# Kernel tuning notes

Hardware: AMD Instinct MI355X
Metric: run time of the kernel (lower is better)

The kernel has to match this reference:

```python
import jax, jax.numpy as jnp
import numpy as np

N_NODES = 100000
N_EDGES = 1600000
S_FEAT = 16   # static node features
D_FEAT = 8    # dynamic node features
E_FEAT = 4    # edge features
K = 2
EDGE_IN = E_FEAT + 2 * S_FEAT + 2 * D_FEAT  # 52
HIDDEN = 2 * D_FEAT                          # 16


def setup_inputs() -> dict:
    key = jax.random.key(0)
    ks = jax.random.split(key, 12)
    inp = {
        "x_s": jax.random.normal(ks[0], (N_NODES, S_FEAT), jnp.float32),
        "x_d": jax.random.normal(ks[1], (N_NODES, D_FEAT), jnp.float32),
        "edge_attr": jax.random.normal(ks[2], (N_EDGES, E_FEAT), jnp.float32),
        # edge MLP: Linear(EDGE_IN->HIDDEN) + ReLU + Linear(HIDDEN->D_FEAT)
        "W1": jax.random.normal(ks[3], (HIDDEN, EDGE_IN), jnp.float32) / np.sqrt(EDGE_IN),
        "b1": jnp.zeros((HIDDEN,), jnp.float32),
        "W2": jax.random.normal(ks[4], (D_FEAT, HIDDEN), jnp.float32) / np.sqrt(HIDDEN),
        "b2": jnp.zeros((D_FEAT,), jnp.float32),
        # K+1 = 3 filter matrices, Linear(D->D, bias=False): y = x @ W.T
        "Wf0": jax.random.normal(ks[5], (D_FEAT, D_FEAT), jnp.float32) / np.sqrt(D_FEAT),
        "Wf1": jax.random.normal(ks[6], (D_FEAT, D_FEAT), jnp.float32) / np.sqrt(D_FEAT),
        "Wf2": jax.random.normal(ks[7], (D_FEAT, D_FEAT), jnp.float32) / np.sqrt(D_FEAT),
        "edge_index": jax.random.randint(ks[8], (2, N_EDGES), 0, N_NODES, jnp.int64
                                         if jax.config.jax_enable_x64 else jnp.int32),
    }
    return inp


def _edge_mlp(e, W1, b1, W2, b2):
    h = jax.nn.relu(e @ W1.T + b1)
    return h @ W2.T + b2


def reference(x_s, x_d, edge_attr, W1, b1, W2, b2, Wf0, Wf1, Wf2, edge_index):
    row, col = edge_index[0], edge_index[1]
    num_nodes = x_d.shape[0]

    # s_ij depends only on static inputs (x_s, x_d, edge_attr), not on `out`,
    # so it is identical across the K steps; compute it once. The per-step
    # boolean edge mask is applied multiplicatively below, which matches the
    # torch masked-gather/scatter exactly (normalization is per-edge).
    e_ij = jnp.concatenate(
        [x_s[row], x_s[col], x_d[row], x_d[col], edge_attr], axis=1)  # [E, 52]
    s_ij = _edge_mlp(e_ij, W1, b1, W2, b2)                            # [E, D]
    nrm = jnp.linalg.norm(s_ij, axis=1, keepdims=True)
    s_ij = jnp.where(nrm > 0, s_ij / jnp.where(nrm > 0, nrm, 1.0), 0.0)

    filters = [Wf0, Wf1, Wf2]
    out = x_d @ filters[0].T
    for k in range(K):
        mask = out.sum(1) != 0                         # [N]
        edge_mask = (mask[row] | mask[col]).astype(out.dtype)  # [E]
        hydraulic_gradient = out[col] - out[row]       # [E, D]
        shift_sum = hydraulic_gradient * s_ij * edge_mask[:, None]
        scattered = jax.ops.segment_sum(shift_sum, col, num_segments=num_nodes)
        scattered = scattered @ filters[k + 1].T
        out = out + scattered
    return out
```

## Files before the change

### kernel.cpp

```cpp
#include <hip/hip_runtime.h>
#include <hip/hip_fp16.h>

#define S_FEAT 16
#define D_FEAT 8
#define E_FEAT 4
#define EDGE_IN 52
#define HIDDEN 16
#define SCAN_CHUNK 2048
#define NSUB 8

typedef unsigned int uint4v __attribute__((ext_vector_type(4)));

__device__ __forceinline__ void mlp_sij(
    const float* __restrict__ x_s, const float* __restrict__ x_d,
    const float* __restrict__ edge_attr,
    const float* __restrict__ W1, const float* __restrict__ b1,
    const float* __restrict__ W2, const float* __restrict__ b2,
    int row, int col, int e, float s[D_FEAT])
{
    float in[EDGE_IN];
    {
        const float4* p = (const float4*)(x_s + (size_t)row * S_FEAT);
#pragma unroll
        for (int q = 0; q < 4; ++q) {
            float4 v = p[q];
            in[q * 4 + 0] = v.x; in[q * 4 + 1] = v.y;
            in[q * 4 + 2] = v.z; in[q * 4 + 3] = v.w;
        }
    }
    {
        const float4* p = (const float4*)(x_s + (size_t)col * S_FEAT);
#pragma unroll
        for (int q = 0; q < 4; ++q) {
            float4 v = p[q];
            in[16 + q * 4 + 0] = v.x; in[16 + q * 4 + 1] = v.y;
            in[16 + q * 4 + 2] = v.z; in[16 + q * 4 + 3] = v.w;
        }
    }
    {
        const float4* p = (const float4*)(x_d + (size_t)row * D_FEAT);
#pragma unroll
        for (int q = 0; q < 2; ++q) {
            float4 v = p[q];
            in[32 + q * 4 + 0] = v.x; in[32 + q * 4 + 1] = v.y;
            in[32 + q * 4 + 2] = v.z; in[32 + q * 4 + 3] = v.w;
        }
    }
    {
        const float4* p = (const float4*)(x_d + (size_t)col * D_FEAT);
#pragma unroll
        for (int q = 0; q < 2; ++q) {
            float4 v = p[q];
            in[40 + q * 4 + 0] = v.x; in[40 + q * 4 + 1] = v.y;
            in[40 + q * 4 + 2] = v.z; in[40 + q * 4 + 3] = v.w;
        }
    }
    {
        float4 v = *(const float4*)(edge_attr + (size_t)e * E_FEAT);
        in[48] = v.x; in[49] = v.y; in[50] = v.z; in[51] = v.w;
    }

    float h[HIDDEN];
#pragma unroll
    for (int i = 0; i < HIDDEN; ++i) {
        float acc = b1[i];
#pragma unroll
        for (int j = 0; j < EDGE_IN; ++j)
            acc = fmaf(in[j], W1[i * EDGE_IN + j], acc);
        h[i] = acc > 0.f ? acc : 0.f;
    }

    float nrm2 = 0.f;
#pragma unroll
    for (int i = 0; i < D_FEAT; ++i) {
        float acc = b2[i];
#pragma unroll
        for (int j = 0; j < HIDDEN; ++j)
            acc = fmaf(h[j], W2[i * HIDDEN + j], acc);
        s[i] = acc;
        nrm2 = fmaf(acc, acc, nrm2);
    }
    float nrm = sqrtf(nrm2);
    float inv = nrm > 0.f ? 1.f / nrm : 0.f;
#pragma unroll
    for (int i = 0; i < D_FEAT; ++i) s[i] *= inv;
}

__device__ __forceinline__ uint4v pack_rec(const float s[8], int row)
{
    int q[8];
#pragma unroll
    for (int i = 0; i < 8; ++i) {
        float v = fminf(fmaxf(s[i] * 2047.f, -2047.f), 2047.f);
        q[i] = (int)rintf(v) & 0xFFF;
    }
    uint4v r;
    r[0] = (unsigned)(q[0] | (q[1] << 12) | (q[2] << 24));
    r[1] = (unsigned)((q[2] >> 8) | (q[3] << 4) | (q[4] << 16) | (q[5] << 28));
    r[2] = (unsigned)((q[5] >> 4) | (q[6] << 8) | (q[7] << 20));
    r[3] = (unsigned)row;
    return r;
}

__device__ __forceinline__ float rec_s(uint4v r, int f)
{
    int off = f * 12;
    unsigned lo = off < 32 ? r[0] : (off < 64 ? r[1] : r[2]);
    unsigned hi = off < 32 ? r[1] : (off < 64 ? r[2] : 0u);
    unsigned sh = (unsigned)off & 31u;
    unsigned long long both = ((unsigned long long)hi << 32) | lo;
    int q = ((int)((unsigned)(both >> sh) << 20)) >> 20;
    return (float)q * (1.f / 2047.f);
}

__device__ __forceinline__ void unpack8h(uint4v w, float* dst)
{
#pragma unroll
    for (int i = 0; i < 4; ++i) {
        unsigned u = w[i];
        __half2 h;
        h = *reinterpret_cast<__half2*>(&u);
        float2 f = __half22float2(h);
        dst[2 * i] = f.x; dst[2 * i + 1] = f.y;
    }
}

__global__ __launch_bounds__(256) void zero_counts_kernel(int* __restrict__ counts, int M)
{
    int i = blockIdx.x * blockDim.x + threadIdx.x;
    if (i < M) counts[i] = 0;
}

__global__ __launch_bounds__(256) void hist_kernel(
    const int* __restrict__ ei, int E, int N, int* __restrict__ counts8)
{
    int e = blockIdx.x * blockDim.x + threadIdx.x;
    if (e >= E) return;
    int col = ei[E + e];
    atomicAdd(&counts8[(threadIdx.x & (NSUB - 1)) * N + col], 1);
}

__global__ __launch_bounds__(256) void scan_local_kernel(
    const int* __restrict__ counts8, int* __restrict__ partial,
    int* __restrict__ blocksums, int N)
{
    __shared__ int sh[256];
    int b = blockIdx.x, t = threadIdx.x;
    int base = b * SCAN_CHUNK + t * 8;
    int v[8];
    int run = 0;
#pragma unroll
    for (int j = 0; j < 8; ++j) {
        int c = 0;
        if (base + j < N) {
#pragma unroll
            for (int s8 = 0; s8 < NSUB; ++s8)
                c += counts8[s8 * N + base + j];
        }
        v[j] = run;
        run += c;
    }
    sh[t] = run;
    __syncthreads();
#pragma unroll
    for (int st = 1; st < 256; st <<= 1) {
        int x = (t >= st) ? sh[t - st] : 0;
        __syncthreads();
        sh[t] += x;
        __syncthreads();
    }
    int excl = sh[t] - run;
    if (t == 255) blocksums[b] = sh[255];
#pragma unroll
    for (int j = 0; j < 8; ++j)
        if (base + j < N) partial[base + j] = excl + v[j];
}

__global__ __launch_bounds__(64) void scan_blk_kernel(int* __restrict__ bs, int NB)
{
    int lane = threadIdx.x;
    int carry = 0;
    for (int base = 0; base < NB; base += 64) {
        int i = base + lane;
        int orig = (i < NB) ? bs[i] : 0;
        int v = orig;
#pragma unroll
        for (int st = 1; st < 64; st <<= 1) {
            int t = __shfl_up(v, st);
            if (lane >= st) v += t;
        }
        if (i < NB) bs[i] = carry + v - orig;
        carry += __shfl(v, 63);
    }
}

__global__ __launch_bounds__(256) void scan_add_kernel(
    int* __restrict__ offsets, int* __restrict__ cursor,
    const int* __restrict__ blocksums, int N, int E)
{
    int i = blockIdx.x * blockDim.x + threadIdx.x;
    if (i < N) {
        int off = offsets[i] + blocksums[i / SCAN_CHUNK];
        offsets[i] = off;
        cursor[i]  = off;
    } else if (i == N) {
        offsets[N] = E;
    }
}

__global__ __launch_bounds__(256) void proj_init_kernel(
    const float* __restrict__ x_s, const float* __restrict__ x_d,
    const float* __restrict__ W1, const float* __restrict__ b1,
    const float* __restrict__ Wf0,
    __half* __restrict__ PRh, __half* __restrict__ PCh,
    float* __restrict__ out, float* __restrict__ S, int N)
{
    int n = blockIdx.x * blockDim.x + threadIdx.x;
    if (n >= N) return;
    float xs[S_FEAT], xd[D_FEAT];
    {
        const float4* p = (const float4*)(x_s + (size_t)n * S_FEAT);
#pragma unroll
        for (int q = 0; q < 4; ++q) {
            float4 v = p[q];
            xs[q * 4 + 0] = v.x; xs[q * 4 + 1] = v.y;
            xs[q * 4 + 2] = v.z; xs[q * 4 + 3] = v.w;
        }
        const float4* pd = (const float4*)(x_d + (size_t)n * D_FEAT);
        float4 a = pd[0], b = pd[1];
        xd[0] = a.x; xd[1] = a.y; xd[2] = a.z; xd[3] = a.w;
        xd[4] = b.x; xd[5] = b.y; xd[6] = b.z; xd[7] = b.w;
    }
    __half prh[HIDDEN], pch[HIDDEN];
#pragma unroll
    for (int i = 0; i < HIDDEN; ++i) {
        const float* w = W1 + i * EDGE_IN;
        float a = b1[i], c = 0.f;
#pragma unroll
        for (int j = 0; j < S_FEAT; ++j) {
            a = fmaf(xs[j], w[j], a);
            c = fmaf(xs[j], w[16 + j], c);
        }
#pragma unroll
        for (int j = 0; j < D_FEAT; ++j) {
            a = fmaf(xd[j], w[32 + j], a);
            c = fmaf(xd[j], w[40 + j], c);
        }
        prh[i] = __float2half_rn(a);
        pch[i] = __float2half_rn(c);
    }
    {
        uint4v* pr = (uint4v*)(PRh + (size_t)n * HIDDEN);
        uint4v* pc = (uint4v*)(PCh + (size_t)n * HIDDEN);
        pr[0] = *(uint4v*)&prh[0]; pr[1] = *(uint4v*)&prh[8];
        pc[0] = *(uint4v*)&pch[0]; pc[1] = *(uint4v*)&pch[8];
    }
    float o[D_FEAT];
    float rs = 0.f;
#pragma unroll
    for (int i = 0; i < D_FEAT; ++i) {
        float acc = 0.f;
#pragma unroll
        for (int j = 0; j < D_FEAT; ++j)
            acc = fmaf(xd[j], Wf0[i * D_FEAT + j], acc);
        o[i] = acc;
        rs += acc;
    }
    float4* op = (float4*)(out + (size_t)n * D_FEAT);
    op[0] = make_float4(o[0], o[1], o[2], o[3]);
    op[1] = make_float4(o[4], o[5], o[6], o[7]);
    S[n] = rs;
}

__global__ __launch_bounds__(256) void mlp_scatter_proj_kernel(
    const __half* __restrict__ PRh, const __half* __restrict__ PCh,
    const float* __restrict__ edge_attr,
    const float* __restrict__ W1,
    const float* __restrict__ W2, const float* __restrict__ b2,
    const int* __restrict__ ei, int E,
    int* __restrict__ cursor, uint4v* __restrict__ recs)
{
    int e = blockIdx.x * blockDim.x + threadIdx.x;
    if (e >= E) return;
    int row = ei[e], col = ei[E + e];

    float pr[HIDDEN], pc[HIDDEN];
    {
        const uint4v* p = (const uint4v*)(PRh + (size_t)row * HIDDEN);
        const uint4v* c = (const uint4v*)(PCh + (size_t)col * HIDDEN);
        uint4v p0 = p[0], p1 = p[1], c0 = c[0], c1 = c[1];
        unpack8h(p0, pr); unpack8h(p1, pr + 8);
        unpack8h(c0, pc); unpack8h(c1, pc + 8);
    }
    float4 ea = *(const float4*)(edge_attr + (size_t)e * E_FEAT);

    float h[HIDDEN];
#pragma unroll
    for (int i = 0; i < HIDDEN; ++i) {
        const float* w = W1 + i * EDGE_IN + 48;
        float acc = pr[i] + pc[i];
        acc = fmaf(ea.x, w[0], acc);
        acc = fmaf(ea.y, w[1], acc);
        acc = fmaf(ea.z, w[2], acc);
        acc = fmaf(ea.w, w[3], acc);
        h[i] = acc > 0.f ? acc : 0.f;
    }

    float s[D_FEAT];
    float nrm2 = 0.f;
#pragma unroll
    for (int i = 0; i < D_FEAT; ++i) {
        float acc = b2[i];
#pragma unroll
        for (int j = 0; j < HIDDEN; ++j)
            acc = fmaf(h[j], W2[i * HIDDEN + j], acc);
        s[i] = acc;
        nrm2 = fmaf(acc, acc, nrm2);
    }
    float nrm = sqrtf(nrm2);
    float inv = nrm > 0.f ? 1.f / nrm : 0.f;
#pragma unroll
    for (int i = 0; i < D_FEAT; ++i) s[i] *= inv;

    uint4v rec = pack_rec(s, row);
    int pos = atomicAdd(&cursor[col], 1);
    __builtin_nontemporal_store(rec, recs + pos);
}

__global__ __launch_bounds__(256) void mlp_scatter_direct_kernel(
    const float* __restrict__ x_s, const float* __restrict__ x_d,
    const float* __restrict__ edge_attr,
    const float* __restrict__ W1, const float* __restrict__ b1,
    const float* __restrict__ W2, const float* __restrict__ b2,
    const int* __restrict__ ei, int E,
    int* __restrict__ cursor, uint4v* __restrict__ recs)
{
    int e = blockIdx.x * blockDim.x + threadIdx.x;
    if (e >= E) return;
    int row = ei[e], col = ei[E + e];
    float s[D_FEAT];
    mlp_sij(x_s, x_d, edge_attr, W1, b1, W2, b2, row, col, e, s);
    uint4v rec = pack_rec(s, row);
    int pos = atomicAdd(&cursor[col], 1);
    __builtin_nontemporal_store(rec, recs + pos);
}

__global__ __launch_bounds__(256) void node_init_kernel(
    const float* __restrict__ x_d, const float* __restrict__ Wf0,
    float* __restrict__ out, float* __restrict__ S, int N)
{
    int n = blockIdx.x * blockDim.x + threadIdx.x;
    if (n >= N) return;
    float xd[D_FEAT];
    const float4* p = (const float4*)(x_d + (size_t)n * D_FEAT);
    float4 a = p[0], b = p[1];
    xd[0] = a.x; xd[1] = a.y; xd[2] = a.z; xd[3] = a.w;
    xd[4] = b.x; xd[5] = b.y; xd[6] = b.z; xd[7] = b.w;
    float o[D_FEAT];
    float rs = 0.f;
#pragma unroll
    for (int i = 0; i < D_FEAT; ++i) {
        float acc = 0.f;
#pragma unroll
        for (int j = 0; j < D_FEAT; ++j)
            acc = fmaf(xd[j], Wf0[i * D_FEAT + j], acc);
        o[i] = acc;
        rs += acc;
    }
    float4* op = (float4*)(out + (size_t)n * D_FEAT);
    op[0] = make_float4(o[0], o[1], o[2], o[3]);
    op[1] = make_float4(o[4], o[5], o[6], o[7]);
    S[n] = rs;
}

__global__ __launch_bounds__(256) void csr_step_kernel(
    const float* __restrict__ out_in, float* __restrict__ out_out,
    const float* __restrict__ S_in, float* __restrict__ S_out,
    const int* __restrict__ offsets, const uint4v* __restrict__ recs,
    const float* __restrict__ Wf, int N)
{
    int lane = threadIdx.x & 63;
    int node = blockIdx.x * 4 + (threadIdx.x >> 6);
    if (node >= N) return;
    int e_sub = lane >> 3, f = lane & 7;
    int beg = offsets[node], end = offsets[node + 1];
    float outc = out_in[(size_t)node * 8 + f];
    bool mc = (S_in[node] != 0.f);
    float acc = 0.f;
    for (int base = beg; base < end; base += 8) {
        int e = base + e_sub;
        bool valid = e < end;
        uint4v rec = (uint4v)(0u);
        if (valid) rec = __builtin_nontemporal_load(recs + e);
        int row = (int)rec[3];
        float s = rec_s(rec, f);
        float outr = out_in[(size_t)row * 8 + f];
        bool m = mc || (S_in[row] != 0.f);
        acc += m ? (outc - outr) * s : 0.f;
    }
    acc += __shfl_xor(acc, 8);
    acc += __shfl_xor(acc, 16);
    acc += __shfl_xor(acc, 32);
    float upd = 0.f;
#pragma unroll
    for (int j = 0; j < 8; ++j) {
        float aj = __shfl(acc, (lane & ~7) | j);
        upd = fmaf(Wf[f * 8 + j], aj, upd);
    }
    float o = outc + upd;
    float rs = o;
    rs += __shfl_xor(rs, 1);
    rs += __shfl_xor(rs, 2);
    rs += __shfl_xor(rs, 4);
    if (e_sub == 0) {
        out_out[(size_t)node * 8 + f] = o;
        if (f == 0) S_out[node] = rs;
    }
}

__global__ __launch_bounds__(256) void fb_node_init_kernel(
    const float* __restrict__ x_d, const float* __restrict__ Wf0,
    float* __restrict__ out, float* __restrict__ scattered, int N)
{
    int n = blockIdx.x * blockDim.x + threadIdx.x;
    if (n >= N) return;
    float xd[D_FEAT];
    const float4* p = (const float4*)(x_d + (size_t)n * D_FEAT);
    float4 a = p[0], b = p[1];
    xd[0] = a.x; xd[1] = a.y; xd[2] = a.z; xd[3] = a.w;
    xd[4] = b.x; xd[5] = b.y; xd[6] = b.z; xd[7] = b.w;
    float o[D_FEAT];
#pragma unroll
    for (int i = 0; i < D_FEAT; ++i) {
        float acc = 0.f;
#pragma unroll
        for (int j = 0; j < D_FEAT; ++j)
            acc = fmaf(xd[j], Wf0[i * D_FEAT + j], acc);
        o[i] = acc;
    }
    float4* op = (float4*)(out + (size_t)n * D_FEAT);
    op[0] = make_float4(o[0], o[1], o[2], o[3]);
    op[1] = make_float4(o[4], o[5], o[6], o[7]);
    float4* sp = (float4*)(scattered + (size_t)n * D_FEAT);
    sp[0] = make_float4(0.f, 0.f, 0.f, 0.f);
    sp[1] = make_float4(0.f, 0.f, 0.f, 0.f);
}

__global__ __launch_bounds__(256) void fb_edge_step_kernel(
    const float* __restrict__ x_s, const float* __restrict__ x_d,
    const float* __restrict__ edge_attr,
    const float* __restrict__ W1, const float* __restrict__ b1,
    const float* __restrict__ W2, const float* __restrict__ b2,
    const float* __restrict__ out,
    const int* __restrict__ ei, int E, float* __restrict__ scattered)
{
    int e = blockIdx.x * blockDim.x + threadIdx.x;
    if (e >= E) return;
    int row = ei[e], col = ei[E + e];
    const float4* pr = (const float4*)(out + (size_t)row * D_FEAT);
    const float4* pc = (const float4*)(out + (size_t)col * D_FEAT);
    float4 r0 = pr[0], r1 = pr[1], c0 = pc[0], c1 = pc[1];
    float srow = r0.x + r0.y + r0.z + r0.w + r1.x + r1.y + r1.z + r1.w;
    float scol = c0.x + c0.y + c0.z + c0.w + c1.x + c1.y + c1.z + c1.w;
    if (srow == 0.f && scol == 0.f) return;
    float s[D_FEAT];
    mlp_sij(x_s, x_d, edge_attr, W1, b1, W2, b2, row, col, e, s);
    float* dst = scattered + (size_t)col * D_FEAT;
    atomicAdd(dst + 0, (c0.x - r0.x) * s[0]);
    atomicAdd(dst + 1, (c0.y - r0.y) * s[1]);
    atomicAdd(dst + 2, (c0.z - r0.z) * s[2]);
    atomicAdd(dst + 3, (c0.w - r0.w) * s[3]);
    atomicAdd(dst + 4, (c1.x - r1.x) * s[4]);
    atomicAdd(dst + 5, (c1.y - r1.y) * s[5]);
    atomicAdd(dst + 6, (c1.z - r1.z) * s[6]);
    atomicAdd(dst + 7, (c1.w - r1.w) * s[7]);
}

__global__ __launch_bounds__(256) void fb_node_update_kernel(
    float* __restrict__ out, float* __restrict__ scattered,
    const float* __restrict__ Wf, int N)
{
    int n = blockIdx.x * blockDim.x + threadIdx.x;
    if (n >= N) return;
    float sc[D_FEAT];
    float4* sp = (float4*)(scattered + (size_t)n * D_FEAT);
    float4 a = sp[0], b = sp[1];
    sc[0] = a.x; sc[1] = a.y; sc[2] = a.z; sc[3] = a.w;
    sc[4] = b.x; sc[5] = b.y; sc[6] = b.z; sc[7] = b.w;
    sp[0] = make_float4(0.f, 0.f, 0.f, 0.f);
    sp[1] = make_float4(0.f, 0.f, 0.f, 0.f);
    float4* op = (float4*)(out + (size_t)n * D_FEAT);
    float4 o0 = op[0], o1 = op[1];
    float o[D_FEAT] = {o0.x, o0.y, o0.z, o0.w, o1.x, o1.y, o1.z, o1.w};
#pragma unroll
    for (int i = 0; i < D_FEAT; ++i) {
        float acc = 0.f;
#pragma unroll
        for (int j = 0; j < D_FEAT; ++j)
            acc = fmaf(sc[j], Wf[i * D_FEAT + j], acc);
        o[i] += acc;
    }
    op[0] = make_float4(o[0], o[1], o[2], o[3]);
    op[1] = make_float4(o[4], o[5], o[6], o[7]);
}

extern "C" void kernel_launch(void* const* d_in, const int* in_sizes, int n_in,
                              void* d_out, int out_size, void* d_ws, size_t ws_size,
                              hipStream_t stream) {
    const float* x_s       = (const float*)d_in[0];
    const float* x_d       = (const float*)d_in[1];
    const float* edge_attr = (const float*)d_in[2];
    const float* W1        = (const float*)d_in[3];
    const float* b1        = (const float*)d_in[4];
    const float* W2        = (const float*)d_in[5];
    const float* b2        = (const float*)d_in[6];
    const float* Wf[3]     = {(const float*)d_in[7], (const float*)d_in[8],
                              (const float*)d_in[9]};
    const int*   ei        = (const int*)d_in[10];

    const int N = in_sizes[1] / D_FEAT;
    const int E = in_sizes[10] / 2;

    float* out = (float*)d_out;

    size_t off = 0;
    auto carve = [&](size_t bytes) { size_t p = off; off = (off + bytes + 255) & ~255ULL; return p; };
    size_t o_counts  = carve((size_t)NSUB * N * 4);
    size_t o_offsets = carve((size_t)(N + 1) * 4);
    size_t o_cursor  = carve((size_t)(N + 1) * 4);
    size_t o_bsums   = carve(256 * 4);
    size_t o_bufA    = carve((size_t)N * D_FEAT * 4);
    size_t o_SA      = carve((size_t)N * 4);
    size_t o_SB      = carve((size_t)N * 4);
    size_t o_recs    = carve((size_t)E * 16);
    const size_t need_base = off;
    size_t o_PR      = carve((size_t)N * HIDDEN * 2);
    size_t o_PC      = carve((size_t)N * HIDDEN * 2);
    const size_t need_full = off;

    dim3 blk(256);
    dim3 gE((E + 255) / 256);
    dim3 gN((N + 255) / 256);

    if (ws_size >= need_base) {
        char* ws = (char*)d_ws;
        int*   counts8 = (int*)(ws + o_counts);
        int*   offsets = (int*)(ws + o_offsets);
        int*   cursor  = (int*)(ws + o_cursor);
        int*   bsums   = (int*)(ws + o_bsums);
        float* bufA    = (float*)(ws + o_bufA);
        float* SA      = (float*)(ws + o_SA);
        float* SB      = (float*)(ws + o_SB);
        uint4v* recs   = (uint4v*)(ws + o_recs);

        const int NB = (N + SCAN_CHUNK - 1) / SCAN_CHUNK;

        zero_counts_kernel<<<dim3((NSUB * N + 255) / 256), blk, 0, stream>>>(counts8, NSUB * N);
        hist_kernel<<<gE, blk, 0, stream>>>(ei, E, N, counts8);
        scan_local_kernel<<<dim3(NB), blk, 0, stream>>>(counts8, offsets, bsums, N);
        scan_blk_kernel<<<dim3(1), dim3(64), 0, stream>>>(bsums, NB);
        scan_add_kernel<<<dim3((N + 256) / 256), blk, 0, stream>>>(offsets, cursor, bsums, N, E);

        if (ws_size >= need_full) {
            __half* PRh = (__half*)(ws + o_PR);
            __half* PCh = (__half*)(ws + o_PC);
            proj_init_kernel<<<gN, blk, 0, stream>>>(
                x_s, x_d, W1, b1, Wf[0], PRh, PCh, out, SA, N);
            mlp_scatter_proj_kernel<<<gE, blk, 0, stream>>>(
                PRh, PCh, edge_attr, W1, W2, b2, ei, E, cursor, recs);
        } else {
            node_init_kernel<<<gN, blk, 0, stream>>>(x_d, Wf[0], out, SA, N);
            mlp_scatter_direct_kernel<<<gE, blk, 0, stream>>>(
                x_s, x_d, edge_attr, W1, b1, W2, b2, ei, E, cursor, recs);
        }

        dim3 gC((N + 3) / 4);
        csr_step_kernel<<<gC, blk, 0, stream>>>(out, bufA, SA, SB, offsets, recs, Wf[1], N);
        csr_step_kernel<<<gC, blk, 0, stream>>>(bufA, out, SB, SA, offsets, recs, Wf[2], N);
    } else {
        float* scattered = (float*)d_ws;
        fb_node_init_kernel<<<gN, blk, 0, stream>>>(x_d, Wf[0], out, scattered, N);
        for (int k = 0; k < 2; ++k) {
            fb_edge_step_kernel<<<gE, blk, 0, stream>>>(
                x_s, x_d, edge_attr, W1, b1, W2, b2, out, ei, E, scattered);
            fb_node_update_kernel<<<gN, blk, 0, stream>>>(out, scattered, Wf[k + 1], N);
        }
    }
}
```

Before: 366.6 us.

## Fuse scan-add into projection, drop row-sum arrays, process two edges per thread

Merges the scan offset finalisation into the node projection kernel, which removes one launch. The S row-sum arrays are dropped, and csr_step now recomputes each node's row sum by shuffling across its 8 feature lanes. The edge MLP/scatter kernel now handles two edges per thread with vectorised nontemporal index loads. Nontemporal loads are also added to the histogram and edge_attr reads. Trade-offs are extra shuffles in the CSR loop and lower thread-level parallelism in the edge kernel.

```diff
diff --git a/kernel.cpp b/kernel.cpp
--- a/kernel.cpp
+++ b/kernel.cpp
@@ -10,6 +10,8 @@
 #define NSUB 8
 
 typedef unsigned int uint4v __attribute__((ext_vector_type(4)));
+typedef float float4v __attribute__((ext_vector_type(4)));
+typedef int int2v __attribute__((ext_vector_type(2)));
 
 __device__ __forceinline__ void mlp_sij(
     const float* __restrict__ x_s, const float* __restrict__ x_d,
@@ -118,8 +120,7 @@
 #pragma unroll
     for (int i = 0; i < 4; ++i) {
         unsigned u = w[i];
-        __half2 h;
-        h = *reinterpret_cast<__half2*>(&u);
+        __half2 h = *reinterpret_cast<__half2*>(&u);
         float2 f = __half22float2(h);
         dst[2 * i] = f.x; dst[2 * i + 1] = f.y;
     }
@@ -136,7 +137,7 @@
 {
     int e = blockIdx.x * blockDim.x + threadIdx.x;
     if (e >= E) return;
-    int col = ei[E + e];
+    int col = __builtin_nontemporal_load(ei + E + e);
     atomicAdd(&counts8[(threadIdx.x & (NSUB - 1)) * N + col], 1);
 }
 
@@ -208,15 +209,23 @@
     }
 }
 
-__global__ __launch_bounds__(256) void proj_init_kernel(
+__global__ __launch_bounds__(256) void proj_scan_kernel(
+    int* __restrict__ offsets, int* __restrict__ cursor,
+    const int* __restrict__ blocksums,
     const float* __restrict__ x_s, const float* __restrict__ x_d,
     const float* __restrict__ W1, const float* __restrict__ b1,
     const float* __restrict__ Wf0,
     __half* __restrict__ PRh, __half* __restrict__ PCh,
-    float* __restrict__ out, float* __restrict__ S, int N)
+    float* __restrict__ out, int N, int E)
 {
     int n = blockIdx.x * blockDim.x + threadIdx.x;
-    if (n >= N) return;
+    if (n > N) return;
+    if (n == N) { offsets[N] = E; return; }
+    {
+        int off = offsets[n] + blocksums[n / SCAN_CHUNK];
+        offsets[n] = off;
+        cursor[n]  = off;
+    }
     float xs[S_FEAT], xd[D_FEAT];
     {
         const float4* p = (const float4*)(x_s + (size_t)n * S_FEAT);
@@ -256,7 +265,6 @@
         pc[0] = *(uint4v*)&pch[0]; pc[1] = *(uint4v*)&pch[8];
     }
     float o[D_FEAT];
-    float rs = 0.f;
 #pragma unroll
     for (int i = 0; i < D_FEAT; ++i) {
         float acc = 0.f;
@@ -264,12 +272,62 @@
         for (int j = 0; j < D_FEAT; ++j)
             acc = fmaf(xd[j], Wf0[i * D_FEAT + j], acc);
         o[i] = acc;
-        rs += acc;
     }
     float4* op = (float4*)(out + (size_t)n * D_FEAT);
     op[0] = make_float4(o[0], o[1], o[2], o[3]);
     op[1] = make_float4(o[4], o[5], o[6], o[7]);
-    S[n] = rs;
+}
+
+__device__ __forceinline__ void edge_work(
+    const __half* __restrict__ PRh, const __half* __restrict__ PCh,
+    const float* __restrict__ edge_attr,
+    const float* __restrict__ W1,
+    const float* __restrict__ W2, const float* __restrict__ b2,
+    int row, int col, int e,
+    int* __restrict__ cursor, uint4v* __restrict__ recs)
+{
+    float pr[HIDDEN], pc[HIDDEN];
+    {
+        const uint4v* p = (const uint4v*)(PRh + (size_t)row * HIDDEN);
+        const uint4v* c = (const uint4v*)(PCh + (size_t)col * HIDDEN);
+        uint4v p0 = p[0], p1 = p[1], c0 = c[0], c1 = c[1];
+        unpack8h(p0, pr); unpack8h(p1, pr + 8);
+        unpack8h(c0, pc); unpack8h(c1, pc + 8);
+    }
+    float4v ea = __builtin_nontemporal_load(
+        (const float4v*)(edge_attr + (size_t)e * E_FEAT));
+
+    float h[HIDDEN];
+#pragma unroll
+    for (int i = 0; i < HIDDEN; ++i) {
+        const float* w = W1 + i * EDGE_IN + 48;
+        float acc = pr[i] + pc[i];
+        acc = fmaf(ea[0], w[0], acc);
+        acc = fmaf(ea[1], w[1], acc);
+        acc = fmaf(ea[2], w[2], acc);
+        acc = fmaf(ea[3], w[3], acc);
+        h[i] = acc > 0.f ? acc : 0.f;
+    }
+
+    float s[D_FEAT];
+    float nrm2 = 0.f;
+#pragma unroll
+    for (int i = 0; i < D_FEAT; ++i) {
+        float acc = b2[i];
+#pragma unroll
+        for (int j = 0; j < HIDDEN; ++j)
+            acc = fmaf(h[j], W2[i * HIDDEN + j], acc);
+        s[i] = acc;
+        nrm2 = fmaf(acc, acc, nrm2);
+    }
+    float nrm = sqrtf(nrm2);
+    float inv = nrm > 0.f ? 1.f / nrm : 0.f;
+#pragma unroll
+    for (int i = 0; i < D_FEAT; ++i) s[i] *= inv;
+
+    uint4v rec = pack_rec(s, row);
+    int pos = atomicAdd(&cursor[col], 1);
+    __builtin_nontemporal_store(rec, recs + pos);
 }
 
 __global__ __launch_bounds__(256) void mlp_scatter_proj_kernel(
@@ -280,51 +338,17 @@
     const int* __restrict__ ei, int E,
     int* __restrict__ cursor, uint4v* __restrict__ recs)
 {
-    int e = blockIdx.x * blockDim.x + threadIdx.x;
-    if (e >= E) return;
-    int row = ei[e], col = ei[E + e];
-
-    float pr[HIDDEN], pc[HIDDEN];
-    {
-        const uint4v* p = (const uint4v*)(PRh + (size_t)row * HIDDEN);
-        const uint4v* c = (const uint4v*)(PCh + (size_t)col * HIDDEN);
-        uint4v p0 = p[0], p1 = p[1], c0 = c[0], c1 = c[1];
-        unpack8h(p0, pr); unpack8h(p1, pr + 8);
-        unpack8h(c0, pc); unpack8h(c1, pc + 8);
-    }
-    float4 ea = *(const float4*)(edge_attr + (size_t)e * E_FEAT);
-
-    float h[HIDDEN];
-#pragma unroll
-    for (int i = 0; i < HIDDEN; ++i) {
-        const float* w = W1 + i * EDGE_IN + 48;
-        float acc = pr[i] + pc[i];
-        acc = fmaf(ea.x, w[0], acc);
-        acc = fmaf(ea.y, w[1], acc);
-        acc = fmaf(ea.z, w[2], acc);
-        acc = fmaf(ea.w, w[3], acc);
-        h[i] = acc > 0.f ? acc : 0.f;
-    }
-
-    float s[D_FEAT];
-    float nrm2 = 0.f;
-#pragma unroll
-    for (int i = 0; i < D_FEAT; ++i) {
-        float acc = b2[i];
-#pragma unroll
-        for (int j = 0; j < HIDDEN; ++j)
-            acc = fmaf(h[j], W2[i * HIDDEN + j], acc);
-        s[i] = acc;
-        nrm2 = fmaf(acc, acc, nrm2);
-    }
-    float nrm = sqrtf(nrm2);
-    float inv = nrm > 0.f ? 1.f / nrm : 0.f;
-#pragma unroll
-    for (int i = 0; i < D_FEAT; ++i) s[i] *= inv;
-
-    uint4v rec = pack_rec(s, row);
-    int pos = atomicAdd(&cursor[col], 1);
-    __builtin_nontemporal_store(rec, recs + pos);
+    int e0 = (blockIdx.x * blockDim.x + threadIdx.x) * 2;
+    if (e0 >= E) return;
+    if (e0 + 1 < E) {
+        int2v rows = __builtin_nontemporal_load((const int2v*)(ei + e0));
+        int2v cols = __builtin_nontemporal_load((const int2v*)(ei + E + e0));
+        edge_work(PRh, PCh, edge_attr, W1, W2, b2, rows[0], cols[0], e0,     cursor, recs);
+        edge_work(PRh, PCh, edge_attr, W1, W2, b2, rows[1], cols[1], e0 + 1, cursor, recs);
+    } else {
+        int row = ei[e0], col = ei[E + e0];
+        edge_work(PRh, PCh, edge_attr, W1, W2, b2, row, col, e0, cursor, recs);
+    }
 }
 
 __global__ __launch_bounds__(256) void mlp_scatter_direct_kernel(
@@ -347,7 +371,7 @@
 
 __global__ __launch_bounds__(256) void node_init_kernel(
     const float* __restrict__ x_d, const float* __restrict__ Wf0,
-    float* __restrict__ out, float* __restrict__ S, int N)
+    float* __restrict__ out, int N)
 {
     int n = blockIdx.x * blockDim.x + threadIdx.x;
     if (n >= N) return;
@@ -357,7 +381,6 @@
     xd[0] = a.x; xd[1] = a.y; xd[2] = a.z; xd[3] = a.w;
     xd[4] = b.x; xd[5] = b.y; xd[6] = b.z; xd[7] = b.w;
     float o[D_FEAT];
-    float rs = 0.f;
 #pragma unroll
     for (int i = 0; i < D_FEAT; ++i) {
         float acc = 0.f;
@@ -365,17 +388,14 @@
         for (int j = 0; j < D_FEAT; ++j)
             acc = fmaf(xd[j], Wf0[i * D_FEAT + j], acc);
         o[i] = acc;
-        rs += acc;
     }
     float4* op = (float4*)(out + (size_t)n * D_FEAT);
     op[0] = make_float4(o[0], o[1], o[2], o[3]);
     op[1] = make_float4(o[4], o[5], o[6], o[7]);
-    S[n] = rs;
 }
 
 __global__ __launch_bounds__(256) void csr_step_kernel(
     const float* __restrict__ out_in, float* __restrict__ out_out,
-    const float* __restrict__ S_in, float* __restrict__ S_out,
     const int* __restrict__ offsets, const uint4v* __restrict__ recs,
     const float* __restrict__ Wf, int N)
 {
@@ -385,7 +405,9 @@
     int e_sub = lane >> 3, f = lane & 7;
     int beg = offsets[node], end = offsets[node + 1];
     float outc = out_in[(size_t)node * 8 + f];
-    bool mc = (S_in[node] != 0.f);
+    float sc = outc;
+    sc += __shfl_xor(sc, 1); sc += __shfl_xor(sc, 2); sc += __shfl_xor(sc, 4);
+    bool mc = (sc != 0.f);
     float acc = 0.f;
     for (int base = beg; base < end; base += 8) {
         int e = base + e_sub;
@@ -395,8 +417,9 @@
         int row = (int)rec[3];
         float s = rec_s(rec, f);
         float outr = out_in[(size_t)row * 8 + f];
-        bool m = mc || (S_in[row] != 0.f);
-        acc += m ? (outc - outr) * s : 0.f;
+        float sr = outr;
+        sr += __shfl_xor(sr, 1); sr += __shfl_xor(sr, 2); sr += __shfl_xor(sr, 4);
+        acc += (mc || sr != 0.f) ? (outc - outr) * s : 0.f;
     }
     acc += __shfl_xor(acc, 8);
     acc += __shfl_xor(acc, 16);
@@ -407,15 +430,8 @@
         float aj = __shfl(acc, (lane & ~7) | j);
         upd = fmaf(Wf[f * 8 + j], aj, upd);
     }
-    float o = outc + upd;
-    float rs = o;
-    rs += __shfl_xor(rs, 1);
-    rs += __shfl_xor(rs, 2);
-    rs += __shfl_xor(rs, 4);
-    if (e_sub == 0) {
-        out_out[(size_t)node * 8 + f] = o;
-        if (f == 0) S_out[node] = rs;
-    }
+    if (e_sub == 0)
+        out_out[(size_t)node * 8 + f] = outc + upd;
 }
 
 __global__ __launch_bounds__(256) void fb_node_init_kernel(
@@ -530,8 +546,6 @@
     size_t o_cursor  = carve((size_t)(N + 1) * 4);
     size_t o_bsums   = carve(256 * 4);
     size_t o_bufA    = carve((size_t)N * D_FEAT * 4);
-    size_t o_SA      = carve((size_t)N * 4);
-    size_t o_SB      = carve((size_t)N * 4);
     size_t o_recs    = carve((size_t)E * 16);
     const size_t need_base = off;
     size_t o_PR      = carve((size_t)N * HIDDEN * 2);
@@ -549,8 +563,6 @@
         int*   cursor  = (int*)(ws + o_cursor);
         int*   bsums   = (int*)(ws + o_bsums);
         float* bufA    = (float*)(ws + o_bufA);
-        float* SA      = (float*)(ws + o_SA);
-        float* SB      = (float*)(ws + o_SB);
         uint4v* recs   = (uint4v*)(ws + o_recs);
 
         const int NB = (N + SCAN_CHUNK - 1) / SCAN_CHUNK;
@@ -559,24 +571,25 @@
         hist_kernel<<<gE, blk, 0, stream>>>(ei, E, N, counts8);
         scan_local_kernel<<<dim3(NB), blk, 0, stream>>>(counts8, offsets, bsums, N);
         scan_blk_kernel<<<dim3(1), dim3(64), 0, stream>>>(bsums, NB);
-        scan_add_kernel<<<dim3((N + 256) / 256), blk, 0, stream>>>(offsets, cursor, bsums, N, E);
 
         if (ws_size >= need_full) {
             __half* PRh = (__half*)(ws + o_PR);
             __half* PCh = (__half*)(ws + o_PC);
-            proj_init_kernel<<<gN, blk, 0, stream>>>(
-                x_s, x_d, W1, b1, Wf[0], PRh, PCh, out, SA, N);
-            mlp_scatter_proj_kernel<<<gE, blk, 0, stream>>>(
+            proj_scan_kernel<<<dim3((N + 256) / 256), blk, 0, stream>>>(
+                offsets, cursor, bsums, x_s, x_d, W1, b1, Wf[0],
+                PRh, PCh, out, N, E);
+            mlp_scatter_proj_kernel<<<dim3((E / 2 + 255) / 256), blk, 0, stream>>>(
                 PRh, PCh, edge_attr, W1, W2, b2, ei, E, cursor, recs);
         } else {
-            node_init_kernel<<<gN, blk, 0, stream>>>(x_d, Wf[0], out, SA, N);
+            scan_add_kernel<<<dim3((N + 256) / 256), blk, 0, stream>>>(offsets, cursor, bsums, N, E);
+            node_init_kernel<<<gN, blk, 0, stream>>>(x_d, Wf[0], out, N);
             mlp_scatter_direct_kernel<<<gE, blk, 0, stream>>>(
                 x_s, x_d, edge_attr, W1, b1, W2, b2, ei, E, cursor, recs);
         }
 
         dim3 gC((N + 3) / 4);
-        csr_step_kernel<<<gC, blk, 0, stream>>>(out, bufA, SA, SB, offsets, recs, Wf[1], N);
-        csr_step_kernel<<<gC, blk, 0, stream>>>(bufA, out, SB, SA, offsets, recs, Wf[2], N);
+        csr_step_kernel<<<gC, blk, 0, stream>>>(out, bufA, offsets, recs, Wf[1], N);
+        csr_step_kernel<<<gC, blk, 0, stream>>>(bufA, out, offsets, recs, Wf[2], N);
     } else {
         float* scattered = (float*)d_ws;
         fb_node_init_kernel<<<gN, blk, 0, stream>>>(x_d, Wf[0], out, scattered, N);
```

New measurement: 375.3 us. 1.02x slower.
